# Kernel optimization log

Hardware: AMD Instinct MI355X
Metric: run time of the kernel (lower is better)

Reference implementation:

```python
import jax, jax.numpy as jnp
import numpy as np
from itertools import combinations_with_replacement

INPUT_LENGTH = 126
ORDER = 3
WEIGHT_DIVISOR = 100
BATCH = 256
N_FEAT = INPUT_LENGTH + 1  # bias term prepended


def setup_inputs() -> dict:
    key = jax.random.key(0)
    kx, kw = jax.random.split(key)
    # exact combination index table, as in HONU._get_combinations
    comb_idx = jnp.asarray(
        np.array(list(combinations_with_replacement(range(N_FEAT), ORDER)), dtype=np.int64)
    )  # [C, ORDER], C = 349504
    num_comb = comb_idx.shape[0]
    x = jax.random.normal(kx, (BATCH, INPUT_LENGTH), dtype=jnp.float32)
    weights = jax.random.uniform(kw, (num_comb,), dtype=jnp.float32) / WEIGHT_DIVISOR
    return {"x": x, "weights": weights, "comb_idx": comb_idx}


def reference(x, weights, comb_idx):
    # prepend bias feature: x_full [B, n_feat]
    ones = jnp.ones((x.shape[0], 1), dtype=x.dtype)
    x_full = jnp.concatenate([ones, x], axis=1)
    # gather feature combinations: [B, C, order]
    selected = jnp.take(x_full, comb_idx, axis=1)
    # monomial products: [B, C]
    colx = jnp.prod(selected, axis=2)
    # weighted sum (GEMV): [B, 1]
    return colx @ weights[:, None]
```

## Files before the change

kernel.cpp:

```cpp
#include <hip/hip_runtime.h>


#define N_FEAT 127
#define C_TOT  349504
#define IN_LEN 126
#define TILE   64
#define NTILES 4
#define NB     192
#define NI     16
#define NTASK  568
#define XPAD   131
#define WROW   128

__device__ __forceinline__ int Foff(int i) {
    const int m = N_FEAT - i;
    return C_TOT - m * (m + 1) * (m + 2) / 6;
}
__device__ __forceinline__ int baseij(int i, int j) {
    return Foff(i) + (j - i) * N_FEAT - ((i + j - 1) * (j - i)) / 2;
}

__global__ __launch_bounds__(256, 3) void honu2(
    const float* __restrict__ x, const float* __restrict__ w,
    float* __restrict__ out)
{
    __shared__ float xS[TILE * XPAD];
    __shared__ float wbuf[NI * WROW];
    __shared__ float red[4 * TILE];

    const int tid  = threadIdx.x;
    const int lane = tid & 63;
    const int wv   = tid >> 6;
    const int tile = blockIdx.y;
    const int g    = blockIdx.x;

    const float* xsrc = x + (size_t)tile * TILE * IN_LEN;
    for (int e = tid; e < TILE * IN_LEN; e += 256) {
        const int r = e / IN_LEN;
        const int c = e - r * IN_LEN;
        xS[r * XPAD + c + 1] = xsrc[e];
    }
    for (int r = tid; r < TILE; r += 256) xS[r * XPAD] = 1.0f;
    for (int e = tid; e < TILE * (XPAD - N_FEAT); e += 256) {
        const int r = e >> 2, c = e & 3;
        xS[r * XPAD + N_FEAT + c] = 0.0f;
    }

    float acc = 0.0f;

    int t = g, jcur = 0, cum = 0;
    while (t < NTASK) {
        int nt_j = (jcur + 1 + NI - 1) >> 4;
        while (cum + nt_j <= t) { cum += nt_j; ++jcur; nt_j = (jcur + 16) >> 4; }
        const int j  = jcur;
        const int i0 = (t - cum) << 4;
        const int k0 = j & ~3;
        const int L4 = (N_FEAT - k0 + 3) & ~3;
        const int nI = min(NI, j + 1 - i0);

        __syncthreads();
        {
            const int kk = tid & 127;
            const int i2 = tid >> 7;
            #pragma unroll
            for (int p = 0; p < NI / 2; ++p) {
                const int ip = i2 + p * 2;
                const int k  = k0 + kk;
                float v = 0.0f;
                if (ip < nI && k >= j && k < N_FEAT)
                    v = w[baseij(i0 + ip, j) + (k - j)];
                wbuf[ip * WROW + kk] = v;
            }
        }
        __syncthreads();

        float d[NI];
        #pragma unroll
        for (int q = 0; q < NI; ++q) d[q] = 0.0f;

        const int KB = L4 >> 2;
        const float* xrow = &xS[lane * XPAD];
        for (int kb = wv; kb < KB; kb += 4) {
            const int kbase = k0 + (kb << 2);
            const float x0 = xrow[kbase + 0];
            const float x1 = xrow[kbase + 1];
            const float x2 = xrow[kbase + 2];
            const float x3 = xrow[kbase + 3];
            #pragma unroll
            for (int q = 0; q < NI; ++q) {
                const float4 w4 = *(const float4*)&wbuf[q * WROW + (kb << 2)];
                d[q] = fmaf(w4.x, x0, d[q]);
                d[q] = fmaf(w4.y, x1, d[q]);
                d[q] = fmaf(w4.z, x2, d[q]);
                d[q] = fmaf(w4.w, x3, d[q]);
            }
        }

        const float xj = xrow[j];
        #pragma unroll
        for (int q = 0; q < NI; ++q) {
            const float xi = xrow[i0 + q];
            acc = fmaf(xi * xj, d[q], acc);
        }
        t += NB;
    }

    red[wv * TILE + lane] = acc;
    __syncthreads();
    if (tid < TILE) {
        const float s = red[tid] + red[TILE + tid] + red[2 * TILE + tid] + red[3 * TILE + tid];
        atomicAdd(&out[tile * TILE + tid], s);
    }
}

extern "C" void kernel_launch(void* const* d_in, const int* in_sizes, int n_in,
                              void* d_out, int out_size, void* d_ws, size_t ws_size,
                              hipStream_t stream)
{
    const float* x = (const float*)d_in[0];
    const float* w = (const float*)d_in[1];
    float* out = (float*)d_out;

    hipMemsetAsync(out, 0, 256 * sizeof(float), stream);
    honu2<<<dim3(NB, NTILES), 256, 0, stream>>>(x, w, out);
}
```

Before: 79.33 us.

## Read weights directly per wave with scalar loads and reduce partials in second kernel

Each wave now takes its own (j, i-block) task of 8 rows and reads weights straight from global memory as wave-uniform vector loads, removing the shared-memory weight staging and the block-wide barriers per task. Partial sums per wave are written to workspace and combined by a separate reduction kernel instead of shared-memory reduction plus atomics. Grid grows to 256 blocks, and tails are handled with a scalar remainder loop and clamped indices. This trades barrier overhead for extra global/scalar cache traffic and an additional kernel launch.

```diff
diff --git a/kernel.cpp b/kernel.cpp
--- a/kernel.cpp
+++ b/kernel.cpp
@@ -6,11 +6,13 @@
 #define IN_LEN 126
 #define TILE   64
 #define NTILES 4
-#define NB     192
-#define NI     16
-#define NTASK  568
-#define XPAD   131
-#define WROW   128
+#define NB     256
+#define NI     8
+#define NTASK  1072
+#define XPAD   127
+#define WPT    (NB * 4)
+
+typedef float f4 __attribute__((ext_vector_type(4), aligned(4)));
 
 __device__ __forceinline__ int Foff(int i) {
     const int m = N_FEAT - i;
@@ -20,17 +22,13 @@
     return Foff(i) + (j - i) * N_FEAT - ((i + j - 1) * (j - i)) / 2;
 }
 
-__global__ __launch_bounds__(256, 3) void honu2(
+__global__ __launch_bounds__(256) void honu3(
     const float* __restrict__ x, const float* __restrict__ w,
-    float* __restrict__ out)
+    float* __restrict__ parts)
 {
     __shared__ float xS[TILE * XPAD];
-    __shared__ float wbuf[NI * WROW];
-    __shared__ float red[4 * TILE];
-
     const int tid  = threadIdx.x;
     const int lane = tid & 63;
-    const int wv   = tid >> 6;
     const int tile = blockIdx.y;
     const int g    = blockIdx.x;
 
@@ -40,77 +38,87 @@
         const int c = e - r * IN_LEN;
         xS[r * XPAD + c + 1] = xsrc[e];
     }
-    for (int r = tid; r < TILE; r += 256) xS[r * XPAD] = 1.0f;
-    for (int e = tid; e < TILE * (XPAD - N_FEAT); e += 256) {
-        const int r = e >> 2, c = e & 3;
-        xS[r * XPAD + N_FEAT + c] = 0.0f;
-    }
+    if (tid < TILE) xS[tid * XPAD] = 1.0f;
+    __syncthreads();
 
+    const int wv = __builtin_amdgcn_readfirstlane(tid >> 6);
+    const float* xrow = &xS[lane * XPAD];
     float acc = 0.0f;
 
-    int t = g, jcur = 0, cum = 0;
-    while (t < NTASK) {
-        int nt_j = (jcur + 1 + NI - 1) >> 4;
-        while (cum + nt_j <= t) { cum += nt_j; ++jcur; nt_j = (jcur + 16) >> 4; }
+    int jcur = 0, cum = 0;
+    for (int t = g * 4 + wv; t < NTASK; t += WPT) {
+        int cnt = (jcur + 8) >> 3;
+        while (cum + cnt <= t) { cum += cnt; ++jcur; cnt = (jcur + 8) >> 3; }
         const int j  = jcur;
-        const int i0 = (t - cum) << 4;
-        const int k0 = j & ~3;
-        const int L4 = (N_FEAT - k0 + 3) & ~3;
-        const int nI = min(NI, j + 1 - i0);
+        const int i0 = (t - cum) << 3;
 
-        __syncthreads();
-        {
-            const int kk = tid & 127;
-            const int i2 = tid >> 7;
-            #pragma unroll
-            for (int p = 0; p < NI / 2; ++p) {
-                const int ip = i2 + p * 2;
-                const int k  = k0 + kk;
-                float v = 0.0f;
-                if (ip < nI && k >= j && k < N_FEAT)
-                    v = w[baseij(i0 + ip, j) + (k - j)];
-                wbuf[ip * WROW + kk] = v;
-            }
-        }
-        __syncthreads();
+        int bq[NI];
+        #pragma unroll
+        for (int q = 0; q < NI; ++q)
+            bq[q] = baseij(min(i0 + q, j), j);
+
+        const int L  = N_FEAT - j;
+        const int KB = L >> 2;
 
         float d[NI];
         #pragma unroll
         for (int q = 0; q < NI; ++q) d[q] = 0.0f;
 
-        const int KB = L4 >> 2;
-        const float* xrow = &xS[lane * XPAD];
-        for (int kb = wv; kb < KB; kb += 4) {
-            const int kbase = k0 + (kb << 2);
-            const float x0 = xrow[kbase + 0];
-            const float x1 = xrow[kbase + 1];
-            const float x2 = xrow[kbase + 2];
-            const float x3 = xrow[kbase + 3];
+        const float* xk = xrow + j;
+        #pragma unroll 2
+        for (int qd = 0; qd < KB; ++qd) {
+            const int kb = qd << 2;
+            f4 w4[NI];
+            #pragma unroll
+            for (int q = 0; q < NI; ++q)
+                w4[q] = *(const f4*)(w + bq[q] + kb);
+            const float x0 = xk[kb + 0], x1 = xk[kb + 1];
+            const float x2 = xk[kb + 2], x3 = xk[kb + 3];
             #pragma unroll
             for (int q = 0; q < NI; ++q) {
-                const float4 w4 = *(const float4*)&wbuf[q * WROW + (kb << 2)];
-                d[q] = fmaf(w4.x, x0, d[q]);
-                d[q] = fmaf(w4.y, x1, d[q]);
-                d[q] = fmaf(w4.z, x2, d[q]);
-                d[q] = fmaf(w4.w, x3, d[q]);
+                d[q] = fmaf(w4[q][0], x0, d[q]);
+                d[q] = fmaf(w4[q][1], x1, d[q]);
+                d[q] = fmaf(w4[q][2], x2, d[q]);
+                d[q] = fmaf(w4[q][3], x3, d[q]);
             }
+        }
+        for (int kk = KB << 2; kk < L; ++kk) {
+            const float xv = xk[kk];
+            #pragma unroll
+            for (int q = 0; q < NI; ++q)
+                d[q] = fmaf(w[bq[q] + kk], xv, d[q]);
         }
 
         const float xj = xrow[j];
         #pragma unroll
         for (int q = 0; q < NI; ++q) {
-            const float xi = xrow[i0 + q];
+            const int iq = i0 + q;
+            const float xv = xrow[min(iq, j)];
+            const float xi = (iq <= j) ? xv : 0.0f;
             acc = fmaf(xi * xj, d[q], acc);
         }
-        t += NB;
     }
 
-    red[wv * TILE + lane] = acc;
-    __syncthreads();
-    if (tid < TILE) {
-        const float s = red[tid] + red[TILE + tid] + red[2 * TILE + tid] + red[3 * TILE + tid];
-        atomicAdd(&out[tile * TILE + tid], s);
+    parts[(size_t)((tile * NB + g) * 4 + wv) * 64 + lane] = acc;
+}
+
+__global__ __launch_bounds__(256) void honu3_reduce(
+    const float* __restrict__ parts, float* __restrict__ out)
+{
+    const int tid  = threadIdx.x;
+    const int lane = tid & 63;
+    const int gg   = tid >> 6;
+    const int tile = blockIdx.x >> 3;
+    const int part = blockIdx.x & 7;
+
+    const float* base = parts + (size_t)tile * WPT * 64;
+    float s = 0.0f;
+    #pragma unroll 8
+    for (int n = 0; n < 32; ++n) {
+        const int wp = part * 128 + (n << 2) + gg;
+        s += base[wp * 64 + lane];
     }
+    atomicAdd(&out[tile * 64 + lane], s);
 }
 
 extern "C" void kernel_launch(void* const* d_in, const int* in_sizes, int n_in,
@@ -119,8 +127,10 @@
 {
     const float* x = (const float*)d_in[0];
     const float* w = (const float*)d_in[1];
-    float* out = (float*)d_out;
+    float* out   = (float*)d_out;
+    float* parts = (float*)d_ws;
 
     hipMemsetAsync(out, 0, 256 * sizeof(float), stream);
-    honu2<<<dim3(NB, NTILES), 256, 0, stream>>>(x, w, out);
+    honu3<<<dim3(NB, NTILES), 256, 0, stream>>>(x, w, parts);
+    honu3_reduce<<<32, 256, 0, stream>>>(parts, out);
 }
```

Measured after the change: 94.06 us. +18.6%, slower.

## Register-tile 4x4 outer product, prefetch weights into registers, balance task assignment

Applied to the files above, without the earlier changes.

Replaces the per-lane 16-dot-product inner loop with a 4x4 register-blocked outer product: each lane handles 4 batch rows and 4 i-rows using vector LDS loads of both x and weights. Weights for the next task are loaded from global into registers while the current task computes, which hides global latency behind math. Tasks are assigned in a folded pattern (g, 383-g, 384+g) and decoded in closed form instead of by a running scan, to balance triangular work across blocks. The final reduction is reorganized to match the new lane-to-row mapping. The cost is more registers and LDS padding changes that could affect occupancy or bank conflicts.

```diff
diff --git a/kernel.cpp b/kernel.cpp
--- a/kernel.cpp
+++ b/kernel.cpp
@@ -4,112 +4,148 @@
 #define N_FEAT 127
 #define C_TOT  349504
 #define IN_LEN 126
-#define TILE   64
 #define NTILES 4
 #define NB     192
-#define NI     16
 #define NTASK  568
-#define XPAD   131
-#define WROW   128
+#define XPAD   132
+#define WROW   132
 
-__device__ __forceinline__ int Foff(int i) {
-    const int m = N_FEAT - i;
-    return C_TOT - m * (m + 1) * (m + 2) / 6;
-}
-__device__ __forceinline__ int baseij(int i, int j) {
-    return Foff(i) + (j - i) * N_FEAT - ((i + j - 1) * (j - i)) / 2;
+typedef float f4 __attribute__((ext_vector_type(4)));
+
+__device__ __forceinline__ int Foff(int i){ const int m = N_FEAT - i; return C_TOT - m*(m+1)*(m+2)/6; }
+__device__ __forceinline__ int baseij(int i,int j){ return Foff(i) + (j-i)*N_FEAT - ((i+j-1)*(j-i))/2; }
+
+__device__ __forceinline__ void decode(int t, int& j, int& i0){
+    int a = (int)((sqrtf(1.0f + 0.5f*(float)t) - 1.0f)*0.5f);
+    if (a < 0) a = 0;
+    while (8*(a+1)*(a+2) <= t) ++a;
+    while (a > 0 && 8*a*(a+1) > t) --a;
+    const int rem = t - 8*a*(a+1);
+    const int ap1 = a + 1;
+    int r = 0;
+    while ((r+1)*ap1 <= rem) ++r;
+    j  = 16*a + r;
+    i0 = (rem - r*ap1) << 4;
 }
 
-__global__ __launch_bounds__(256, 3) void honu2(
-    const float* __restrict__ x, const float* __restrict__ w,
-    float* __restrict__ out)
+__global__ __launch_bounds__(256, 3) void honu4(
+    const float* __restrict__ x, const float* __restrict__ w, float* __restrict__ out)
 {
-    __shared__ float xS[TILE * XPAD];
-    __shared__ float wbuf[NI * WROW];
-    __shared__ float red[4 * TILE];
+    __shared__ float smem[64*XPAD + 16*WROW];
+    float* xS = smem;
+    float* wb = smem + 64*XPAD;
 
     const int tid  = threadIdx.x;
     const int lane = tid & 63;
     const int wv   = tid >> 6;
+    const int m    = lane & 15;
+    const int gq   = lane >> 4;
     const int tile = blockIdx.y;
     const int g    = blockIdx.x;
 
-    const float* xsrc = x + (size_t)tile * TILE * IN_LEN;
-    for (int e = tid; e < TILE * IN_LEN; e += 256) {
-        const int r = e / IN_LEN;
-        const int c = e - r * IN_LEN;
-        xS[r * XPAD + c + 1] = xsrc[e];
+    const float* xsrc = x + (size_t)tile * 64 * IN_LEN;
+    for (int e = tid; e < 64*IN_LEN; e += 256){
+        const int r = e / IN_LEN, c = e - r*IN_LEN;
+        xS[r*XPAD + c + 1] = xsrc[e];
     }
-    for (int r = tid; r < TILE; r += 256) xS[r * XPAD] = 1.0f;
-    for (int e = tid; e < TILE * (XPAD - N_FEAT); e += 256) {
-        const int r = e >> 2, c = e & 3;
-        xS[r * XPAD + N_FEAT + c] = 0.0f;
+    if (tid < 64) xS[tid*XPAD] = 1.0f;
+    for (int e = tid; e < 64*5; e += 256){
+        const int r = e/5, c = e - r*5;
+        xS[r*XPAD + 127 + c] = 0.0f;
     }
 
-    float acc = 0.0f;
+    float acc[4] = {0.f, 0.f, 0.f, 0.f};
 
-    int t = g, jcur = 0, cum = 0;
-    while (t < NTASK) {
-        int nt_j = (jcur + 1 + NI - 1) >> 4;
-        while (cum + nt_j <= t) { cum += nt_j; ++jcur; nt_j = (jcur + 16) >> 4; }
-        const int j  = jcur;
-        const int i0 = (t - cum) << 4;
-        const int k0 = j & ~3;
-        const int L4 = (N_FEAT - k0 + 3) & ~3;
-        const int nI = min(NI, j + 1 - i0);
+    int tl[3];
+    tl[0] = g; tl[1] = 383 - g; tl[2] = 384 + g;
+    const int ntl = (384 + g < NTASK) ? 3 : 2;
+
+    const int sm4 = tid & 127;
+    const int ss0 = tid >> 7;
+
+    int pj=0, pi0=0, pk0=0, pQ=0, pnI=0;
+    bool have = false;
+
+    for (int ti = 0; ti <= ntl; ++ti) {
+        float rv[8] = {0.f,0.f,0.f,0.f,0.f,0.f,0.f,0.f};
+        int cj=0, ci0=0, ck0=0, cQ=0, cnI=0;
+        if (ti < ntl) {
+            decode(tl[ti], cj, ci0);
+            ck0 = cj & ~3;
+            cQ  = (N_FEAT - ck0 + 3) >> 2;
+            cnI = min(16, cj + 1 - ci0);
+            const int dj = cj - ck0;
+            #pragma unroll
+            for (int p = 0; p < 8; ++p) {
+                const int s = ss0 + 2*p;
+                if (s < cnI && sm4 >= dj && ck0 + sm4 < N_FEAT)
+                    rv[p] = w[baseij(ci0 + s, cj) + (ck0 + sm4 - cj)];
+            }
+        }
+
+        if (have) {
+            f4 dd[4];
+            #pragma unroll
+            for (int qq=0; qq<4; ++qq) dd[qq] = (f4){0.f,0.f,0.f,0.f};
+
+            for (int q8 = wv; q8 < pQ; q8 += 4) {
+                const int m4 = q8 << 2;
+                f4 xq[4], wq[4];
+                #pragma unroll
+                for (int rr=0; rr<4; ++rr)
+                    xq[rr] = *(const f4*)&xS[(m + 16*rr)*XPAD + pk0 + m4];
+                #pragma unroll
+                for (int qq=0; qq<4; ++qq)
+                    wq[qq] = *(const f4*)&wb[(gq + 4*qq)*WROW + m4];
+                #pragma unroll
+                for (int qq=0; qq<4; ++qq){
+                    #pragma unroll
+                    for (int rr=0; rr<4; ++rr){
+                        dd[qq][rr] = fmaf(wq[qq][0], xq[rr][0], dd[qq][rr]);
+                        dd[qq][rr] = fmaf(wq[qq][1], xq[rr][1], dd[qq][rr]);
+                        dd[qq][rr] = fmaf(wq[qq][2], xq[rr][2], dd[qq][rr]);
+                        dd[qq][rr] = fmaf(wq[qq][3], xq[rr][3], dd[qq][rr]);
+                    }
+                }
+            }
+            #pragma unroll
+            for (int rr=0; rr<4; ++rr){
+                const float* xr = &xS[(m + 16*rr)*XPAD];
+                const float xj = xr[pj];
+                float a = 0.f;
+                #pragma unroll
+                for (int qq=0; qq<4; ++qq){
+                    const int s = gq + 4*qq;
+                    const float xi = (s < pnI) ? xr[pi0 + s] : 0.0f;
+                    a = fmaf(xi, dd[qq][rr], a);
+                }
+                acc[rr] = fmaf(xj, a, acc[rr]);
+            }
+        }
 
         __syncthreads();
-        {
-            const int kk = tid & 127;
-            const int i2 = tid >> 7;
+        if (ti < ntl) {
             #pragma unroll
-            for (int p = 0; p < NI / 2; ++p) {
-                const int ip = i2 + p * 2;
-                const int k  = k0 + kk;
-                float v = 0.0f;
-                if (ip < nI && k >= j && k < N_FEAT)
-                    v = w[baseij(i0 + ip, j) + (k - j)];
-                wbuf[ip * WROW + kk] = v;
-            }
+            for (int p = 0; p < 8; ++p)
+                wb[(ss0 + 2*p)*WROW + sm4] = rv[p];
         }
         __syncthreads();
 
-        float d[NI];
-        #pragma unroll
-        for (int q = 0; q < NI; ++q) d[q] = 0.0f;
-
-        const int KB = L4 >> 2;
-        const float* xrow = &xS[lane * XPAD];
-        for (int kb = wv; kb < KB; kb += 4) {
-            const int kbase = k0 + (kb << 2);
-            const float x0 = xrow[kbase + 0];
-            const float x1 = xrow[kbase + 1];
-            const float x2 = xrow[kbase + 2];
-            const float x3 = xrow[kbase + 3];
-            #pragma unroll
-            for (int q = 0; q < NI; ++q) {
-                const float4 w4 = *(const float4*)&wbuf[q * WROW + (kb << 2)];
-                d[q] = fmaf(w4.x, x0, d[q]);
-                d[q] = fmaf(w4.y, x1, d[q]);
-                d[q] = fmaf(w4.z, x2, d[q]);
-                d[q] = fmaf(w4.w, x3, d[q]);
-            }
-        }
-
-        const float xj = xrow[j];
-        #pragma unroll
-        for (int q = 0; q < NI; ++q) {
-            const float xi = xrow[i0 + q];
-            acc = fmaf(xi * xj, d[q], acc);
-        }
-        t += NB;
+        pj=cj; pi0=ci0; pk0=ck0; pQ=cQ; pnI=cnI; have = (ti < ntl);
     }
 
-    red[wv * TILE + lane] = acc;
+    float* red = wb;
+    *(f4*)&red[tid*4] = (f4){acc[0], acc[1], acc[2], acc[3]};
     __syncthreads();
-    if (tid < TILE) {
-        const float s = red[tid] + red[TILE + tid] + red[2 * TILE + tid] + red[3 * TILE + tid];
-        atomicAdd(&out[tile * TILE + tid], s);
+    if (tid < 64) {
+        const int mm = tid & 15, rr = tid >> 4;
+        float s = 0.f;
+        #pragma unroll
+        for (int u = 0; u < 16; ++u) {
+            const int src = (u >> 2)*64 + (u & 3)*16 + mm;
+            s += red[src*4 + rr];
+        }
+        atomicAdd(&out[tile*64 + tid], s);
     }
 }
 
@@ -122,5 +158,5 @@
     float* out = (float*)d_out;
 
     hipMemsetAsync(out, 0, 256 * sizeof(float), stream);
-    honu2<<<dim3(NB, NTILES), 256, 0, stream>>>(x, w, out);
+    honu4<<<dim3(NB, NTILES), 256, 0, stream>>>(x, w, out);
 }
```

Result: faster. 74.82 us (-5.7%).
